# Performance work log

Hardware: AMD Instinct MI355X
Metric: run time of the kernel (lower is better)

The kernel has to match this reference:

```python
import jax, jax.numpy as jnp
import numpy as np

IN_DIM = 256
OUT_DIM = 256

def setup_inputs() -> dict:
    key = jax.random.key(0)
    k1, k2, k3, k4 = jax.random.split(key, 4)
    B, N, K, D = 4, 10000, 16, IN_DIM
    x = jax.random.normal(k1, (B, N, D), dtype=jnp.float32)
    neigh = jax.random.randint(k2, (N, K), 0, N, dtype=jnp.int64)
    # nn.Linear(2*in_dim, out_dim): W [out, 2*in], b [out]
    bound = 1.0 / np.sqrt(2 * D)
    W = jax.random.uniform(k3, (OUT_DIM, 2 * D), minval=-bound, maxval=bound, dtype=jnp.float32)
    b = jax.random.uniform(k4, (OUT_DIM,), minval=-bound, maxval=bound, dtype=jnp.float32)
    return {"x": x, "neigh": neigh, "W": W, "b": b}

def reference(x, neigh, W, b):
    # x: [B,N,D], neigh: [N,K] with -1 = padding
    mask = (neigh >= 0)                                # [N,K]
    idx = jnp.clip(neigh, 0, None)                     # [N,K]
    # batch_gather_nodes: x_nei[b,n,k,:] = x[b, idx[n,k], :]
    x_nei = x[:, idx, :]                               # [B,N,K,D]
    x_nei = x_nei * mask[None, :, :, None].astype(x.dtype)
    denom = jnp.clip(mask.sum(axis=1), 1, None).astype(x.dtype)  # [N]
    agg = x_nei.sum(axis=2) / denom[None, :, None]     # [B,N,D]
    h = jnp.concatenate([x, agg], axis=-1)             # [B,N,2D]
    return jax.nn.relu(jnp.einsum('bnd,od->bno', h, W) + b)
```

## Files before the change

### kernel.cpp

```cpp
#include <hip/hip_runtime.h>
#include <hip/hip_bf16.h>
#include <stdint.h>

#define B_   4
#define N_   10000
#define K_   16
#define D_   256
#define OUT_ 256
#define KDIM 512
#define M_   (B_ * N_)
#define CW   32
#define NCH  8
#define CHUNK_ELEMS ((size_t)N_ * B_ * CW)

typedef __attribute__((ext_vector_type(8))) short          short8;
typedef __attribute__((ext_vector_type(8))) unsigned short ushort8;
typedef __attribute__((ext_vector_type(4))) float          f32x4;
typedef __attribute__((ext_vector_type(4))) unsigned short ushort4_t;

__device__ inline unsigned short f2bf(float f) {
    __hip_bfloat16 h = __float2bfloat16(f);
    return *reinterpret_cast<unsigned short*>(&h);
}
__device__ inline float bf2f(unsigned short u) {
    unsigned int v = ((unsigned int)u) << 16;
    return __builtin_bit_cast(float, v);
}

__global__ __launch_bounds__(256) void prep(const float* __restrict__ x,
                                            const float* __restrict__ W,
                                            unsigned short* __restrict__ xc,
                                            unsigned short* __restrict__ Wb) {
    const int t = threadIdx.x;
    if (blockIdx.x < 5000) {
        const int n  = blockIdx.x * 2 + (t >> 7);
        const int b  = (t >> 5) & 3;
        const int c0 = (t & 31) * 8;
        const float4* xr = (const float4*)(x + ((size_t)b * N_ + n) * D_ + c0);
        float4 v0 = xr[0];
        float4 v1 = xr[1];
        ushort8 s;
        s[0] = f2bf(v0.x); s[1] = f2bf(v0.y); s[2] = f2bf(v0.z); s[3] = f2bf(v0.w);
        s[4] = f2bf(v1.x); s[5] = f2bf(v1.y); s[6] = f2bf(v1.z); s[7] = f2bf(v1.w);
        const int ch  = c0 >> 5;
        const int col = c0 & 31;
        *(ushort8*)(xc + (size_t)ch * CHUNK_ELEMS + ((size_t)n * B_ + b) * CW + col) = s;
    } else {
        int g = (blockIdx.x - 5000) * 256 + t;
        float4 v = ((const float4*)W)[g];
        ushort4_t s;
        s.x = f2bf(v.x); s.y = f2bf(v.y); s.z = f2bf(v.z); s.w = f2bf(v.w);
        ((ushort4_t*)Wb)[g] = s;
    }
}

__global__ __launch_bounds__(256) void gather_agg(const unsigned short* __restrict__ xc,
                                                  const int*            __restrict__ neigh,
                                                  unsigned short*       __restrict__ hagg) {
    const int c   = blockIdx.x & 7;
    const int g   = blockIdx.x >> 3;
    const int n0  = g * 8;
    const int tid = threadIdx.x;

    __shared__ int   idx_s[8 * K_];
    __shared__ float inv_s[8];

    if (tid < 8 * K_) idx_s[tid] = neigh[n0 * K_ + tid];
    __syncthreads();
    if (tid < 8) {
        int cnt = 0;
#pragma unroll
        for (int k = 0; k < K_; ++k) cnt += idx_s[tid * K_ + k] >= 0 ? 1 : 0;
        inv_s[tid] = 1.0f / (float)(cnt > 1 ? cnt : 1);
    }
    __syncthreads();

    const int q  = tid & 7;
    const int tl = tid >> 3;
    const int ns = tl >> 2;
    const int b  = tl & 3;

    const unsigned short* xcc = xc + (size_t)c * CHUNK_ELEMS;

    int jj[K_];
#pragma unroll
    for (int k = 0; k < K_; ++k) jj[k] = idx_s[ns * K_ + k];

    ushort4_t vv[K_];
#pragma unroll
    for (int k = 0; k < K_; ++k) {
        const int jc = jj[k] >= 0 ? jj[k] : 0;
        vv[k] = *(const ushort4_t*)(xcc + ((size_t)jc * B_ + b) * CW + q * 4);
    }

    float a0 = 0.f, a1 = 0.f, a2 = 0.f, a3 = 0.f;
#pragma unroll
    for (int k = 0; k < K_; ++k) {
        const float m = jj[k] >= 0 ? 1.f : 0.f;
        a0 += bf2f(vv[k].x) * m;
        a1 += bf2f(vv[k].y) * m;
        a2 += bf2f(vv[k].z) * m;
        a3 += bf2f(vv[k].w) * m;
    }
    const float inv = inv_s[ns];

    ushort4_t s;
    s.x = f2bf(a0 * inv); s.y = f2bf(a1 * inv);
    s.z = f2bf(a2 * inv); s.w = f2bf(a3 * inv);
    *(ushort4_t*)(hagg + ((size_t)b * N_ + n0 + ns) * D_ + c * CW + q * 4) = s;
}

__global__ __launch_bounds__(256) void gemm_bt3(const unsigned short* __restrict__ xc,
                                                const unsigned short* __restrict__ hagg,
                                                const unsigned short* __restrict__ Bm,
                                                const float* __restrict__ bias,
                                                float* __restrict__ out) {
    __shared__ unsigned short As[64 * 32];
    __shared__ unsigned short Bs[256 * 32];

    const int tid    = threadIdx.x;
    const int w      = tid >> 6;
    const int lane   = tid & 63;
    const int tile_m = blockIdx.x * 64;
    const int q      = lane >> 4;
    const int r16    = lane & 15;

    const int crow = lane >> 2;
    const int kofs = (lane & 3) * 8;

    const unsigned short* ps[4];
    const unsigned short* pa[4];
#pragma unroll
    for (int c = 0; c < 4; ++c) {
        const int m  = tile_m + c * 16 + crow;
        const int b  = (m >= N_) + (m >= 2 * N_) + (m >= 3 * N_);
        const int n  = m - b * N_;
        ps[c] = xc + ((size_t)n * B_ + b) * CW + kofs;
        pa[c] = hagg + (size_t)m * D_ + kofs;
    }

    f32x4 acc[4][4] = {};

    for (int kk = 0; kk < KDIM; kk += 32) {
        const int kidx = kk >> 5;
#pragma unroll
        for (int t = 0; t < 5; ++t) {
            const int c = w * 5 + t;
            if (c < 4) {
                const unsigned short* ga = (kk < D_)
                    ? ps[c] + (size_t)kidx * CHUNK_ELEMS
                    : pa[c] + (kk - D_);
                __builtin_amdgcn_global_load_lds(
                    (const __attribute__((address_space(1))) void*)ga,
                    (__attribute__((address_space(3))) void*)(As + c * 512),
                    16, 0, 0);
            } else {
                const int row = (c - 4) * 16 + crow;
                const unsigned short* gb = Bm + (size_t)row * KDIM + kk + kofs;
                __builtin_amdgcn_global_load_lds(
                    (const __attribute__((address_space(1))) void*)gb,
                    (__attribute__((address_space(3))) void*)(Bs + (c - 4) * 512),
                    16, 0, 0);
            }
        }
        __syncthreads();

        short8 a[4], bf[4];
#pragma unroll
        for (int i = 0; i < 4; ++i)
            a[i] = *(const short8*)(As + (i * 16 + r16) * 32 + q * 8);
#pragma unroll
        for (int j = 0; j < 4; ++j)
            bf[j] = *(const short8*)(Bs + (w * 64 + j * 16 + r16) * 32 + q * 8);

#pragma unroll
        for (int i = 0; i < 4; ++i)
#pragma unroll
            for (int j = 0; j < 4; ++j)
                acc[i][j] = __builtin_amdgcn_mfma_f32_16x16x32_bf16(a[i], bf[j], acc[i][j], 0, 0, 0);

        __syncthreads();
    }

    float bj[4];
#pragma unroll
    for (int j = 0; j < 4; ++j)
        bj[j] = bias[w * 64 + j * 16 + r16];

#pragma unroll
    for (int i = 0; i < 4; ++i) {
#pragma unroll
        for (int reg = 0; reg < 4; ++reg) {
            const int m = tile_m + i * 16 + q * 4 + reg;
            float* orow = out + (size_t)m * OUT_ + w * 64;
#pragma unroll
            for (int j = 0; j < 4; ++j) {
                float v = acc[i][j][reg] + bj[j];
                orow[j * 16 + r16] = v > 0.f ? v : 0.f;
            }
        }
    }
}

extern "C" void kernel_launch(void* const* d_in, const int* in_sizes, int n_in,
                              void* d_out, int out_size, void* d_ws, size_t ws_size,
                              hipStream_t stream) {
    const float* x     = (const float*)d_in[0];
    const int*   neigh = (const int*)d_in[1];
    const float* W     = (const float*)d_in[2];
    const float* bias  = (const float*)d_in[3];
    float*       out   = (float*)d_out;

    unsigned short* Wb   = (unsigned short*)d_ws;
    unsigned short* xc   = Wb + OUT_ * KDIM;
    unsigned short* hagg = xc + NCH * CHUNK_ELEMS;

    prep<<<5000 + 128, 256, 0, stream>>>(x, W, xc, Wb);
    gather_agg<<<(N_ / 8) * NCH, 256, 0, stream>>>(xc, neigh, hagg);
    gemm_bt3<<<M_ / 64, 256, 0, stream>>>(xc, hagg, Wb, bias, out);
}
```

Before: 138.6 us.

## Retile GEMM to 128x128 blocks with 2x2 warp grid and K=64 steps

The GEMM moves from 64-row by 256-column tiles to 128x128 tiles laid out on a 2D grid, so each of the four warps computes a 64x64 sub-tile in a 2x2 arrangement. Each iteration now loads a K-slice of 64, split into two 32-wide halves loaded by different warps, which halves the number of barrier pairs. Loading is split by role: two warps load A and two load B. The aim is a more balanced A/B reuse per block and less sync overhead, at the cost of a ragged last M tile that needs clamping and guarded stores, and twice as many blocks along N.

```diff
diff --git a/kernel.cpp b/kernel.cpp
--- a/kernel.cpp
+++ b/kernel.cpp
@@ -110,93 +110,106 @@
     *(ushort4_t*)(hagg + ((size_t)b * N_ + n0 + ns) * D_ + c * CW + q * 4) = s;
 }
 
-__global__ __launch_bounds__(256) void gemm_bt3(const unsigned short* __restrict__ xc,
+__global__ __launch_bounds__(256) void gemm_bt4(const unsigned short* __restrict__ xc,
                                                 const unsigned short* __restrict__ hagg,
                                                 const unsigned short* __restrict__ Bm,
                                                 const float* __restrict__ bias,
                                                 float* __restrict__ out) {
-    __shared__ unsigned short As[64 * 32];
-    __shared__ unsigned short Bs[256 * 32];
+    __shared__ unsigned short As[2 * 128 * 32];
+    __shared__ unsigned short Bs[2 * 128 * 32];
 
     const int tid    = threadIdx.x;
     const int w      = tid >> 6;
     const int lane   = tid & 63;
-    const int tile_m = blockIdx.x * 64;
+    const int tile_m = blockIdx.x * 128;
+    const int nt     = blockIdx.y;
+    const int wm     = w & 1;
+    const int wn     = w >> 1;
     const int q      = lane >> 4;
     const int r16    = lane & 15;
 
     const int crow = lane >> 2;
     const int kofs = (lane & 3) * 8;
 
-    const unsigned short* ps[4];
-    const unsigned short* pa[4];
-#pragma unroll
-    for (int c = 0; c < 4; ++c) {
-        const int m  = tile_m + c * 16 + crow;
-        const int b  = (m >= N_) + (m >= 2 * N_) + (m >= 3 * N_);
-        const int n  = m - b * N_;
+    const unsigned short* ps[8];
+    const unsigned short* pa[8];
+    const unsigned short* pb[8];
+#pragma unroll
+    for (int c = 0; c < 8; ++c) {
+        int m = tile_m + c * 16 + crow;
+        if (m > M_ - 1) m = M_ - 1;
+        const int b = (m >= N_) + (m >= 2 * N_) + (m >= 3 * N_);
+        const int n = m - b * N_;
         ps[c] = xc + ((size_t)n * B_ + b) * CW + kofs;
         pa[c] = hagg + (size_t)m * D_ + kofs;
+        pb[c] = Bm + (size_t)(nt * 128 + c * 16 + crow) * KDIM + kofs;
     }
 
     f32x4 acc[4][4] = {};
 
-    for (int kk = 0; kk < KDIM; kk += 32) {
-        const int kidx = kk >> 5;
-#pragma unroll
-        for (int t = 0; t < 5; ++t) {
-            const int c = w * 5 + t;
-            if (c < 4) {
-                const unsigned short* ga = (kk < D_)
-                    ? ps[c] + (size_t)kidx * CHUNK_ELEMS
-                    : pa[c] + (kk - D_);
+    for (int it = 0; it < 8; ++it) {
+        const int kk = it * 64;
+        if (w < 2) {
+            const int kks = kk + w * 32;
+#pragma unroll
+            for (int c = 0; c < 8; ++c) {
+                const unsigned short* ga = (kks < D_)
+                    ? ps[c] + (size_t)(kks >> 5) * CHUNK_ELEMS
+                    : pa[c] + (kks - D_);
                 __builtin_amdgcn_global_load_lds(
                     (const __attribute__((address_space(1))) void*)ga,
-                    (__attribute__((address_space(3))) void*)(As + c * 512),
+                    (__attribute__((address_space(3))) void*)(As + w * 4096 + c * 512),
                     16, 0, 0);
-            } else {
-                const int row = (c - 4) * 16 + crow;
-                const unsigned short* gb = Bm + (size_t)row * KDIM + kk + kofs;
+            }
+        } else {
+            const int kks = kk + (w - 2) * 32;
+#pragma unroll
+            for (int c = 0; c < 8; ++c) {
+                const unsigned short* gb = pb[c] + kks;
                 __builtin_amdgcn_global_load_lds(
                     (const __attribute__((address_space(1))) void*)gb,
-                    (__attribute__((address_space(3))) void*)(Bs + (c - 4) * 512),
+                    (__attribute__((address_space(3))) void*)(Bs + (w - 2) * 4096 + c * 512),
                     16, 0, 0);
             }
         }
         __syncthreads();
 
-        short8 a[4], bf[4];
-#pragma unroll
-        for (int i = 0; i < 4; ++i)
-            a[i] = *(const short8*)(As + (i * 16 + r16) * 32 + q * 8);
-#pragma unroll
-        for (int j = 0; j < 4; ++j)
-            bf[j] = *(const short8*)(Bs + (w * 64 + j * 16 + r16) * 32 + q * 8);
-
-#pragma unroll
-        for (int i = 0; i < 4; ++i)
+#pragma unroll
+        for (int sub = 0; sub < 2; ++sub) {
+            short8 a[4], bf[4];
+#pragma unroll
+            for (int i = 0; i < 4; ++i)
+                a[i] = *(const short8*)(As + sub * 4096 + (wm * 64 + i * 16 + r16) * 32 + q * 8);
 #pragma unroll
             for (int j = 0; j < 4; ++j)
-                acc[i][j] = __builtin_amdgcn_mfma_f32_16x16x32_bf16(a[i], bf[j], acc[i][j], 0, 0, 0);
-
+                bf[j] = *(const short8*)(Bs + sub * 4096 + (wn * 64 + j * 16 + r16) * 32 + q * 8);
+
+#pragma unroll
+            for (int i = 0; i < 4; ++i)
+#pragma unroll
+                for (int j = 0; j < 4; ++j)
+                    acc[i][j] = __builtin_amdgcn_mfma_f32_16x16x32_bf16(a[i], bf[j], acc[i][j], 0, 0, 0);
+        }
         __syncthreads();
     }
 
     float bj[4];
 #pragma unroll
     for (int j = 0; j < 4; ++j)
-        bj[j] = bias[w * 64 + j * 16 + r16];
+        bj[j] = bias[nt * 128 + wn * 64 + j * 16 + r16];
 
 #pragma unroll
     for (int i = 0; i < 4; ++i) {
 #pragma unroll
         for (int reg = 0; reg < 4; ++reg) {
-            const int m = tile_m + i * 16 + q * 4 + reg;
-            float* orow = out + (size_t)m * OUT_ + w * 64;
-#pragma unroll
-            for (int j = 0; j < 4; ++j) {
-                float v = acc[i][j][reg] + bj[j];
-                orow[j * 16 + r16] = v > 0.f ? v : 0.f;
+            const int m = tile_m + wm * 64 + i * 16 + q * 4 + reg;
+            if (m < M_) {
+                float* orow = out + (size_t)m * OUT_ + nt * 128 + wn * 64;
+#pragma unroll
+                for (int j = 0; j < 4; ++j) {
+                    float v = acc[i][j][reg] + bj[j];
+                    orow[j * 16 + r16] = v > 0.f ? v : 0.f;
+                }
             }
         }
     }
@@ -217,5 +230,5 @@
 
     prep<<<5000 + 128, 256, 0, stream>>>(x, W, xc, Wb);
     gather_agg<<<(N_ / 8) * NCH, 256, 0, stream>>>(xc, neigh, hagg);
-    gemm_bt3<<<M_ / 64, 256, 0, stream>>>(xc, hagg, Wb, bias, out);
-}
+    gemm_bt4<<<dim3((M_ + 127) / 128, OUT_ / 128), 256, 0, stream>>>(xc, hagg, Wb, bias, out);
+}
```

Result: slower. 147.7 us (+6.6%).
